# Kernel optimization log

Hardware: AMD Instinct MI355X
Metric: run time of the kernel (lower is better)

The kernel has to match this reference:

```python
import jax, jax.numpy as jnp
import numpy as np

THRESHOLD = 0.3
STRENGTH = 0.1
MIN_S = 0.0
MAX_S = 0.5
EPS_COS = 1e-8
EPS_LN = 1e-5

B, T, D = 1024, 64, 256
P = 2048
H = 512


def _layernorm(x, g, b):
    mu = x.mean(-1, keepdims=True)
    var = ((x - mu) ** 2).mean(-1, keepdims=True)
    return (x - mu) * jax.lax.rsqrt(var + EPS_LN) * g + b


def setup_inputs() -> dict:
    key = jax.random.key(0)
    ks = jax.random.split(key, 10)
    s = lambda fan_in: 1.0 / np.sqrt(fan_in)
    return {
        "current_feat": jax.random.normal(ks[0], (B, T, D), jnp.float32),
        "prototype": jax.random.normal(ks[1], (P, T, D), jnp.float32),
        "dd_w1": jax.random.normal(ks[2], (2 * D, H), jnp.float32) * s(2 * D),
        "dd_b1": jnp.zeros((H,), jnp.float32),
        "dd_g1": jnp.ones((H,), jnp.float32),
        "dd_be1": jnp.zeros((H,), jnp.float32),
        "dd_w2": jax.random.normal(ks[3], (H, H // 2), jnp.float32) * s(H),
        "dd_b2": jnp.zeros((H // 2,), jnp.float32),
        "dd_w3": jax.random.normal(ks[4], (H // 2, 1), jnp.float32) * s(H // 2),
        "dd_b3": jnp.zeros((1,), jnp.float32),
        "cal_w1": jax.random.normal(ks[5], (D, H), jnp.float32) * s(D),
        "cal_b1": jnp.zeros((H,), jnp.float32),
        "cal_g1": jnp.ones((H,), jnp.float32),
        "cal_be1": jnp.zeros((H,), jnp.float32),
        "cal_w2": jax.random.normal(ks[6], (H, H), jnp.float32) * s(H),
        "cal_b2": jnp.zeros((H,), jnp.float32),
        "cal_w3": jax.random.normal(ks[7], (H, D), jnp.float32) * s(H),
        "cal_b3": jnp.zeros((D,), jnp.float32),
    }


def reference(current_feat, prototype,
              dd_w1, dd_b1, dd_g1, dd_be1, dd_w2, dd_b2, dd_w3, dd_b3,
              cal_w1, cal_b1, cal_g1, cal_be1, cal_w2, cal_b2, cal_w3, cal_b3):
    # --- drift detection ---
    feat_flat = current_feat.mean(axis=1)          # [B, D]
    proto_centers = prototype.mean(axis=1)         # [P, D]
    fn = jnp.maximum(jnp.linalg.norm(feat_flat, axis=-1), EPS_COS)   # [B]
    pn = jnp.maximum(jnp.linalg.norm(proto_centers, axis=-1), EPS_COS)  # [P]
    sim = jnp.einsum('bd,pd->bp', feat_flat, proto_centers) / (fn[:, None] * pn[None, :])
    drift_score = 1.0 - sim                        # [B, P]
    is_drifted = drift_score.mean(axis=0) > THRESHOLD  # [P] bool

    # --- calibration (batched over all P, then masked scatter) ---
    global_mean = feat_flat.mean(axis=0)           # [D]
    concat = jnp.concatenate(
        [proto_centers, jnp.broadcast_to(global_mean, (proto_centers.shape[0], global_mean.shape[0]))], axis=-1)  # [P, 2D]
    h = jax.nn.relu(_layernorm(concat @ dd_w1 + dd_b1, dd_g1, dd_be1))
    h = jax.nn.relu(h @ dd_w2 + dd_b2)
    drift_conf = jax.nn.sigmoid(h @ dd_w3 + dd_b3)[:, 0]  # [P]

    c = jax.nn.relu(_layernorm(proto_centers @ cal_w1 + cal_b1, cal_g1, cal_be1))
    c = jax.nn.relu(c @ cal_w2 + cal_b2)
    delta = c @ cal_w3 + cal_b3                    # [P, D]

    strength = jnp.clip(STRENGTH * drift_conf, MIN_S, MAX_S)  # [P]
    new_center = proto_centers + strength[:, None] * delta    # [P, D]

    calibrated = jnp.where(is_drifted[:, None, None], new_center[:, None, :], prototype)  # [P, T, D]
    return calibrated, drift_score, is_drifted
```

## Files before the change

kernel.cpp:

```cpp
#include <hip/hip_runtime.h>
#include <hip/hip_bf16.h>
#include <math.h>

#define BB 1024
#define TT 64
#define DD 256
#define PP 2048
#define HH 512

typedef __attribute__((ext_vector_type(8))) short short8;
typedef __attribute__((ext_vector_type(4))) float f32x4;

__device__ __forceinline__ float blk_reduce(float v, float* sm) {
    int tid = threadIdx.x;
    #pragma unroll
    for (int o = 32; o > 0; o >>= 1) v += __shfl_down(v, o, 64);
    if ((tid & 63) == 0) sm[tid >> 6] = v;
    __syncthreads();
    float r = sm[0] + sm[1] + sm[2] + sm[3];
    __syncthreads();
    return r;
}

__device__ __forceinline__ float row_mean_vec(const float* __restrict__ base,
                                              float* __restrict__ smr) {
    int tid = threadIdx.x;
    int c4 = tid & 63;
    int t0 = tid >> 6;
    float4 s = make_float4(0.f, 0.f, 0.f, 0.f);
    #pragma unroll
    for (int t = t0; t < TT; t += 4) {
        float4 v = *(const float4*)(base + t * DD + (c4 << 2));
        s.x += v.x; s.y += v.y; s.z += v.z; s.w += v.w;
    }
    *(float4*)&smr[t0 * 256 + (c4 << 2)] = s;
    __syncthreads();
    float m = (smr[tid] + smr[256 + tid] + smr[512 + tid] + smr[768 + tid]) * (1.f / TT);
    __syncthreads();
    return m;
}

__global__ void prep_k(const float* __restrict__ cf, const float* __restrict__ proto,
                       const float* __restrict__ dd_w1, const float* __restrict__ dd_w2,
                       const float* __restrict__ cal_w1, const float* __restrict__ cal_w2,
                       const float* __restrict__ cal_w3,
                       float* __restrict__ gmean8, float* __restrict__ fn,
                       float* __restrict__ pn, float* __restrict__ pc,
                       __hip_bfloat16* __restrict__ ffb, __hip_bfloat16* __restrict__ pcb,
                       __hip_bfloat16* __restrict__ w1cat, __hip_bfloat16* __restrict__ w2dd,
                       __hip_bfloat16* __restrict__ w2cal, __hip_bfloat16* __restrict__ w3cal) {
    __shared__ float smr[1024];
    __shared__ float sm[4];
    int b = blockIdx.x, tid = threadIdx.x;
    if (b < 1024) {
        float m = row_mean_vec(cf + (size_t)b * TT * DD, smr);
        ffb[(size_t)b * DD + tid] = __float2bfloat16(m);
        atomicAdd(&gmean8[(b & 7) * 256 + tid], m * (1.f / BB));
        float tot = blk_reduce(m * m, sm);
        if (tid == 0) fn[b] = fmaxf(sqrtf(tot), 1e-8f);
    } else if (b < 3072) {
        int r = b - 1024;
        float m = row_mean_vec(proto + (size_t)r * TT * DD, smr);
        pc[(size_t)r * DD + tid] = m;
        pcb[(size_t)r * DD + tid] = __float2bfloat16(m);
        float tot = blk_reduce(m * m, sm);
        if (tid == 0) pn[r] = fmaxf(sqrtf(tot), 1e-8f);
    } else {
        int idx = (b - 3072) * 256 + tid;
        if (idx < 262144) {
            int half = idx >> 17;
            int i = idx & 131071;
            int n = i & 511, k = i >> 9;
            const float* src = half ? cal_w1 : dd_w1;
            w1cat[(size_t)(half * 512 + n) * 256 + k] = __float2bfloat16(src[(size_t)k * 512 + n]);
        } else if (idx < 393216) {
            int i = idx - 262144;
            int n = i & 255, k = i >> 8;
            w2dd[(size_t)n * 512 + k] = __float2bfloat16(dd_w2[(size_t)k * 256 + n]);
        } else if (idx < 655360) {
            int i = idx - 393216;
            int n = i & 511, k = i >> 9;
            w2cal[(size_t)n * 512 + k] = __float2bfloat16(cal_w2[(size_t)k * 512 + n]);
        } else {
            int i = idx - 655360;
            int n = i & 255, k = i >> 8;
            w3cal[(size_t)n * 512 + k] = __float2bfloat16(cal_w3[(size_t)k * 256 + n]);
        }
    }
}

__global__ void sim_addvec_k(const __hip_bfloat16* __restrict__ A,
                             const __hip_bfloat16* __restrict__ Bt,
                             const float* __restrict__ fn, const float* __restrict__ pn,
                             const float* __restrict__ gmean8,
                             const float* __restrict__ dd_w1, const float* __restrict__ dd_b1,
                             float* __restrict__ drift, float* __restrict__ colsum,
                             float* __restrict__ addvec) {
    if (blockIdx.x >= 512) {
        __shared__ float gmk[256];
        int tid = threadIdx.x;
        float g = 0.f;
        #pragma unroll
        for (int s = 0; s < 8; ++s) g += gmean8[s * 256 + tid];
        gmk[tid] = g;
        __syncthreads();
        int j = (blockIdx.x - 512) * 256 + tid;
        float s = dd_b1[j];
        #pragma unroll 8
        for (int k = 0; k < 256; ++k) s = fmaf(gmk[k], dd_w1[(size_t)(256 + k) * 512 + j], s);
        addvec[j] = s;
        return;
    }
    int wid = (blockIdx.x << 2) + (threadIdx.x >> 6);
    int lane = threadIdx.x & 63;
    int mw = wid >> 6, nw = wid & 63;
    int m0 = mw << 5, n0 = nw << 5;
    int lr = lane & 15, quad = lane >> 4;
    const __hip_bfloat16* pa0 = A + (size_t)(m0 + lr) * DD + quad * 8;
    const __hip_bfloat16* pa1 = pa0 + 16 * DD;
    const __hip_bfloat16* pb0 = Bt + (size_t)(n0 + lr) * DD + quad * 8;
    const __hip_bfloat16* pb1 = pb0 + 16 * DD;
    f32x4 acc00 = {0,0,0,0}, acc01 = {0,0,0,0}, acc10 = {0,0,0,0}, acc11 = {0,0,0,0};
    #pragma unroll
    for (int k = 0; k < DD; k += 32) {
        short8 a0 = *(const short8*)(pa0 + k);
        short8 a1 = *(const short8*)(pa1 + k);
        short8 b0 = *(const short8*)(pb0 + k);
        short8 b1 = *(const short8*)(pb1 + k);
        acc00 = __builtin_amdgcn_mfma_f32_16x16x32_bf16(a0, b0, acc00, 0, 0, 0);
        acc01 = __builtin_amdgcn_mfma_f32_16x16x32_bf16(a0, b1, acc01, 0, 0, 0);
        acc10 = __builtin_amdgcn_mfma_f32_16x16x32_bf16(a1, b0, acc10, 0, 0, 0);
        acc11 = __builtin_amdgcn_mfma_f32_16x16x32_bf16(a1, b1, acc11, 0, 0, 0);
    }
    int col0 = n0 + lr, col1 = col0 + 16;
    float ip0 = 1.f / pn[col0], ip1 = 1.f / pn[col1];
    float cs0 = 0.f, cs1 = 0.f;
    #pragma unroll
    for (int r = 0; r < 4; ++r) {
        int row0 = m0 + quad * 4 + r;
        int row1 = row0 + 16;
        float if0 = 1.f / fn[row0];
        float if1 = 1.f / fn[row1];
        float d00 = 1.f - acc00[r] * if0 * ip0;
        float d01 = 1.f - acc01[r] * if0 * ip1;
        float d10 = 1.f - acc10[r] * if1 * ip0;
        float d11 = 1.f - acc11[r] * if1 * ip1;
        drift[(size_t)row0 * PP + col0] = d00;
        drift[(size_t)row0 * PP + col1] = d01;
        drift[(size_t)row1 * PP + col0] = d10;
        drift[(size_t)row1 * PP + col1] = d11;
        cs0 += d00 + d10;
        cs1 += d01 + d11;
    }
    cs0 += __shfl_xor(cs0, 16, 64); cs0 += __shfl_xor(cs0, 32, 64);
    cs1 += __shfl_xor(cs1, 16, 64); cs1 += __shfl_xor(cs1, 32, 64);
    if (quad == 0) {
        atomicAdd(&colsum[col0], cs0);
        atomicAdd(&colsum[col1], cs1);
    }
}

template <int K, int OUT_BF16, int RELU>
__device__ __forceinline__ void gemm_tile(const __hip_bfloat16* __restrict__ A,
                                          const __hip_bfloat16* __restrict__ Bt,
                                          const float* __restrict__ bias0,
                                          const float* __restrict__ bias1, int split,
                                          void* __restrict__ Cout, int N, int lognt,
                                          int wid, int lane) {
    int mw = wid >> lognt, nw = wid & ((1 << lognt) - 1);
    int m0 = mw << 5, n0 = nw << 5;
    int lr = lane & 15, quad = lane >> 4;
    const __hip_bfloat16* pa0 = A + (size_t)(m0 + lr) * K + quad * 8;
    const __hip_bfloat16* pa1 = pa0 + 16 * K;
    const __hip_bfloat16* pb0 = Bt + (size_t)(n0 + lr) * K + quad * 8;
    const __hip_bfloat16* pb1 = pb0 + 16 * K;
    f32x4 acc00 = {0,0,0,0}, acc01 = {0,0,0,0}, acc10 = {0,0,0,0}, acc11 = {0,0,0,0};
    #pragma unroll
    for (int k = 0; k < K; k += 32) {
        short8 a0 = *(const short8*)(pa0 + k);
        short8 a1 = *(const short8*)(pa1 + k);
        short8 b0 = *(const short8*)(pb0 + k);
        short8 b1 = *(const short8*)(pb1 + k);
        acc00 = __builtin_amdgcn_mfma_f32_16x16x32_bf16(a0, b0, acc00, 0, 0, 0);
        acc01 = __builtin_amdgcn_mfma_f32_16x16x32_bf16(a0, b1, acc01, 0, 0, 0);
        acc10 = __builtin_amdgcn_mfma_f32_16x16x32_bf16(a1, b0, acc10, 0, 0, 0);
        acc11 = __builtin_amdgcn_mfma_f32_16x16x32_bf16(a1, b1, acc11, 0, 0, 0);
    }
    int col0 = n0 + lr, col1 = col0 + 16;
    float bi0 = (col0 < split) ? bias0[col0] : bias1[col0 - split];
    float bi1 = (col1 < split) ? bias0[col1] : bias1[col1 - split];
    #pragma unroll
    for (int r = 0; r < 4; ++r) {
        int row0 = m0 + quad * 4 + r;
        int row1 = row0 + 16;
        float v00 = acc00[r] + bi0, v01 = acc01[r] + bi1;
        float v10 = acc10[r] + bi0, v11 = acc11[r] + bi1;
        if (RELU) {
            v00 = fmaxf(v00, 0.f); v01 = fmaxf(v01, 0.f);
            v10 = fmaxf(v10, 0.f); v11 = fmaxf(v11, 0.f);
        }
        if (OUT_BF16) {
            __hip_bfloat16* C = (__hip_bfloat16*)Cout;
            C[(size_t)row0 * N + col0] = __float2bfloat16(v00);
            C[(size_t)row0 * N + col1] = __float2bfloat16(v01);
            C[(size_t)row1 * N + col0] = __float2bfloat16(v10);
            C[(size_t)row1 * N + col1] = __float2bfloat16(v11);
        } else {
            float* C = (float*)Cout;
            C[(size_t)row0 * N + col0] = v00;
            C[(size_t)row0 * N + col1] = v01;
            C[(size_t)row1 * N + col0] = v10;
            C[(size_t)row1 * N + col1] = v11;
        }
    }
}

__global__ void gemm1_k(const __hip_bfloat16* __restrict__ pcb,
                        const __hip_bfloat16* __restrict__ w1cat,
                        const float* __restrict__ addvec, const float* __restrict__ cal_b1,
                        float* __restrict__ buf1) {
    int wid = (blockIdx.x << 2) + (threadIdx.x >> 6);
    gemm_tile<256, 0, 0>(pcb, w1cat, addvec, cal_b1, 512, buf1, 1024, 5,
                         wid, threadIdx.x & 63);
}

__global__ void ln2_k(const float* __restrict__ X,
                      __hip_bfloat16* __restrict__ Ydd, __hip_bfloat16* __restrict__ Ycal,
                      const float* __restrict__ gdd, const float* __restrict__ bedd,
                      const float* __restrict__ gcal, const float* __restrict__ becal) {
    __shared__ float sm[4];
    int r = blockIdx.x, tid = threadIdx.x;
    const float* row = X + (size_t)r * 1024;
    {
        float x0 = row[tid], x1 = row[tid + 256];
        float mu = blk_reduce(x0 + x1, sm) * (1.f / HH);
        float d0 = x0 - mu, d1 = x1 - mu;
        float var = blk_reduce(d0 * d0 + d1 * d1, sm) * (1.f / HH);
        float rs = rsqrtf(var + 1e-5f);
        __hip_bfloat16* y = Ydd + (size_t)r * HH;
        y[tid]       = __float2bfloat16(fmaxf(d0 * rs * gdd[tid] + bedd[tid], 0.f));
        y[tid + 256] = __float2bfloat16(fmaxf(d1 * rs * gdd[tid + 256] + bedd[tid + 256], 0.f));
    }
    {
        float x0 = row[512 + tid], x1 = row[768 + tid];
        float mu = blk_reduce(x0 + x1, sm) * (1.f / HH);
        float d0 = x0 - mu, d1 = x1 - mu;
        float var = blk_reduce(d0 * d0 + d1 * d1, sm) * (1.f / HH);
        float rs = rsqrtf(var + 1e-5f);
        __hip_bfloat16* y = Ycal + (size_t)r * HH;
        y[tid]       = __float2bfloat16(fmaxf(d0 * rs * gcal[tid] + becal[tid], 0.f));
        y[tid + 256] = __float2bfloat16(fmaxf(d1 * rs * gcal[tid + 256] + becal[tid + 256], 0.f));
    }
}

__global__ void gemm2_k(const __hip_bfloat16* __restrict__ act_dd,
                        const __hip_bfloat16* __restrict__ act_cal,
                        const __hip_bfloat16* __restrict__ w2dd,
                        const __hip_bfloat16* __restrict__ w2cal,
                        const float* __restrict__ dd_b2, const float* __restrict__ cal_b2,
                        __hip_bfloat16* __restrict__ act2b, __hip_bfloat16* __restrict__ act3b) {
    int lane = threadIdx.x & 63;
    if (blockIdx.x < 128) {
        int wid = (blockIdx.x << 2) + (threadIdx.x >> 6);
        gemm_tile<512, 1, 1>(act_dd, w2dd, dd_b2, dd_b2, 1 << 30, act2b, 256, 3, wid, lane);
    } else {
        int wid = ((blockIdx.x - 128) << 2) + (threadIdx.x >> 6);
        gemm_tile<512, 1, 1>(act_cal, w2cal, cal_b2, cal_b2, 1 << 30, act3b, 512, 4, wid, lane);
    }
}

__global__ void gemm3_conf_k(const __hip_bfloat16* __restrict__ act3b,
                             const __hip_bfloat16* __restrict__ w3cal,
                             const float* __restrict__ cal_b3,
                             const __hip_bfloat16* __restrict__ act2b,
                             const float* __restrict__ dd_w3, const float* __restrict__ dd_b3,
                             const float* __restrict__ colsum,
                             float* __restrict__ delta, float* __restrict__ strength,
                             float* __restrict__ out_is) {
    if (blockIdx.x < 128) {
        int wid = (blockIdx.x << 2) + (threadIdx.x >> 6);
        gemm_tile<512, 0, 0>(act3b, w3cal, cal_b3, cal_b3, 1 << 30, delta, 256, 3,
                             wid, threadIdx.x & 63);
        return;
    }
    int p = ((blockIdx.x - 128) << 2) + (threadIdx.x >> 6);
    int lane = threadIdx.x & 63;
    const __hip_bfloat16* row = act2b + (size_t)p * 256 + lane * 4;
    float s = 0.f;
    #pragma unroll
    for (int j = 0; j < 4; ++j)
        s += __bfloat162float(row[j]) * dd_w3[lane * 4 + j];
    #pragma unroll
    for (int o = 32; o > 0; o >>= 1) s += __shfl_down(s, o, 64);
    if (lane == 0) {
        float conf = 1.f / (1.f + expf(-(s + dd_b3[0])));
        strength[p] = fminf(fmaxf(0.1f * conf, 0.f), 0.5f);
        out_is[p] = (colsum[p] * (1.f / BB) > 0.3f) ? 1.f : 0.f;
    }
}

__global__ void finalize_k(const float* __restrict__ pc, const float* __restrict__ delta,
                           const float* __restrict__ strength, const float* __restrict__ colsum,
                           const float* __restrict__ proto, float* __restrict__ out) {
    int p = blockIdx.x;
    int d4 = (threadIdx.x & 63) << 2;
    int t0 = threadIdx.x >> 6;
    bool dr = colsum[p] * (1.f / BB) > 0.3f;
    float* o = out + (size_t)p * TT * DD;
    if (dr) {
        float s = strength[p];
        float4 pcv = *(const float4*)(pc + (size_t)p * DD + d4);
        float4 dv  = *(const float4*)(delta + (size_t)p * DD + d4);
        float4 nc = make_float4(fmaf(s, dv.x, pcv.x), fmaf(s, dv.y, pcv.y),
                                fmaf(s, dv.z, pcv.z), fmaf(s, dv.w, pcv.w));
        #pragma unroll
        for (int t = t0; t < TT; t += 4)
            *(float4*)(o + t * DD + d4) = nc;
    } else {
        const float* pr = proto + (size_t)p * TT * DD;
        #pragma unroll
        for (int t = t0; t < TT; t += 4)
            *(float4*)(o + t * DD + d4) = *(const float4*)(pr + t * DD + d4);
    }
}

extern "C" void kernel_launch(void* const* d_in, const int* in_sizes, int n_in,
                              void* d_out, int out_size, void* d_ws, size_t ws_size,
                              hipStream_t stream) {
    const float* cf     = (const float*)d_in[0];
    const float* proto  = (const float*)d_in[1];
    const float* dd_w1  = (const float*)d_in[2];
    const float* dd_b1  = (const float*)d_in[3];
    const float* dd_g1  = (const float*)d_in[4];
    const float* dd_be1 = (const float*)d_in[5];
    const float* dd_w2  = (const float*)d_in[6];
    const float* dd_b2  = (const float*)d_in[7];
    const float* dd_w3  = (const float*)d_in[8];
    const float* dd_b3  = (const float*)d_in[9];
    const float* cal_w1 = (const float*)d_in[10];
    const float* cal_b1 = (const float*)d_in[11];
    const float* cal_g1 = (const float*)d_in[12];
    const float* cal_be1= (const float*)d_in[13];
    const float* cal_w2 = (const float*)d_in[14];
    const float* cal_b2 = (const float*)d_in[15];
    const float* cal_w3 = (const float*)d_in[16];
    const float* cal_b3 = (const float*)d_in[17];

    float* out_cal   = (float*)d_out;
    float* out_drift = out_cal + (size_t)PP * TT * DD;
    float* out_is    = out_drift + (size_t)BB * PP;

    float* w = (float*)d_ws;
    float* gmean8   = w;
    float* colsum   = w + 2048;
    float* addvec   = w + 4096;
    float* fn       = w + 4608;
    float* pn       = w + 5632;
    float* strength = w + 7680;
    float* pc       = w + 9728;
    float* buf1     = w + 534016;
    float* delta    = w + 2631168;
    __hip_bfloat16* bb = (__hip_bfloat16*)(w + 3155456);
    __hip_bfloat16* ffb     = bb;
    __hip_bfloat16* pcb     = bb + 262144;
    __hip_bfloat16* w1cat   = bb + 786432;
    __hip_bfloat16* w2dd    = bb + 1048576;
    __hip_bfloat16* w2cal   = bb + 1179648;
    __hip_bfloat16* w3cal   = bb + 1441792;
    __hip_bfloat16* act_dd  = bb + 1572864;
    __hip_bfloat16* act_cal = bb + 2621440;
    __hip_bfloat16* act2b   = bb + 3670016;
    __hip_bfloat16* act3b   = bb + 4194304;

    hipMemsetAsync(d_ws, 0, 4096 * sizeof(float), stream);

    prep_k<<<6144, 256, 0, stream>>>(cf, proto, dd_w1, dd_w2, cal_w1, cal_w2, cal_w3,
                                     gmean8, fn, pn, pc, ffb, pcb,
                                     w1cat, w2dd, w2cal, w3cal);
    sim_addvec_k<<<514, 256, 0, stream>>>(ffb, pcb, fn, pn, gmean8, dd_w1, dd_b1,
                                          out_drift, colsum, addvec);
    gemm1_k<<<512, 256, 0, stream>>>(pcb, w1cat, addvec, cal_b1, buf1);
    ln2_k<<<PP, 256, 0, stream>>>(buf1, act_dd, act_cal, dd_g1, dd_be1, cal_g1, cal_be1);
    gemm2_k<<<384, 256, 0, stream>>>(act_dd, act_cal, w2dd, w2cal, dd_b2, cal_b2,
                                     act2b, act3b);
    gemm3_conf_k<<<640, 256, 0, stream>>>(act3b, w3cal, cal_b3, act2b, dd_w3, dd_b3,
                                          colsum, delta, strength, out_is);
    finalize_k<<<PP, 256, 0, stream>>>(pc, delta, strength, colsum, proto, out_cal);
}
```

Measured before the change: 415.7 us.

## Batch row-mean loads, drop gmean atomics, use nontemporal stores, single-pass LayerNorm

Row-mean loads are issued all at once (16 float4 per thread) to raise memory-level parallelism. The global-mean atomics are replaced by storing per-row means and having the addvec blocks reduce them directly. Drift and calibrated-output writes become nontemporal stores to avoid polluting cache. LayerNorm now computes mean and variance in one fused reduction (E[x^2]-mu^2), which is slightly less numerically stable. Together these cut atomic traffic, sync points and cache pressure in a bandwidth-bound pipeline.

Measured after the change: 410.2 us. No clear change (-1.3%).

```diff
diff --git a/kernel.cpp b/kernel.cpp
--- a/kernel.cpp
+++ b/kernel.cpp
@@ -10,6 +10,19 @@
 
 typedef __attribute__((ext_vector_type(8))) short short8;
 typedef __attribute__((ext_vector_type(4))) float f32x4;
+
+__device__ __forceinline__ float4 f4add(float4 a, float4 b) {
+    return make_float4(a.x + b.x, a.y + b.y, a.z + b.z, a.w + b.w);
+}
+
+__device__ __forceinline__ void nt_store4(float* p, float4 v) {
+    f32x4 t = {v.x, v.y, v.z, v.w};
+    __builtin_nontemporal_store(t, (f32x4*)p);
+}
+
+__device__ __forceinline__ void nt_store1(float* p, float v) {
+    __builtin_nontemporal_store(v, p);
+}
 
 __device__ __forceinline__ float blk_reduce(float v, float* sm) {
     int tid = threadIdx.x;
@@ -22,29 +35,46 @@
     return r;
 }
 
-__device__ __forceinline__ float row_mean_vec(const float* __restrict__ base,
-                                              float* __restrict__ smr) {
+__device__ __forceinline__ float2 blk_reduce2(float a, float b, float* sm) {
+    int tid = threadIdx.x;
+    #pragma unroll
+    for (int o = 32; o > 0; o >>= 1) {
+        a += __shfl_down(a, o, 64);
+        b += __shfl_down(b, o, 64);
+    }
+    if ((tid & 63) == 0) { sm[(tid >> 6) * 2] = a; sm[(tid >> 6) * 2 + 1] = b; }
+    __syncthreads();
+    float ra = sm[0] + sm[2] + sm[4] + sm[6];
+    float rb = sm[1] + sm[3] + sm[5] + sm[7];
+    __syncthreads();
+    return make_float2(ra, rb);
+}
+
+__device__ __forceinline__ float row_mean_batch(const float* __restrict__ base,
+                                                float* __restrict__ smr) {
     int tid = threadIdx.x;
     int c4 = tid & 63;
     int t0 = tid >> 6;
-    float4 s = make_float4(0.f, 0.f, 0.f, 0.f);
-    #pragma unroll
-    for (int t = t0; t < TT; t += 4) {
-        float4 v = *(const float4*)(base + t * DD + (c4 << 2));
-        s.x += v.x; s.y += v.y; s.z += v.z; s.w += v.w;
-    }
+    const float* p = base + t0 * DD + (c4 << 2);
+    float4 v[16];
+    #pragma unroll
+    for (int i = 0; i < 16; ++i)
+        v[i] = *(const float4*)(p + (i << 2) * DD);
+    #pragma unroll
+    for (int i = 0; i < 8; ++i) v[i] = f4add(v[i], v[i + 8]);
+    #pragma unroll
+    for (int i = 0; i < 4; ++i) v[i] = f4add(v[i], v[i + 4]);
+    float4 s = f4add(f4add(v[0], v[1]), f4add(v[2], v[3]));
     *(float4*)&smr[t0 * 256 + (c4 << 2)] = s;
     __syncthreads();
-    float m = (smr[tid] + smr[256 + tid] + smr[512 + tid] + smr[768 + tid]) * (1.f / TT);
-    __syncthreads();
-    return m;
+    return (smr[tid] + smr[256 + tid] + smr[512 + tid] + smr[768 + tid]) * (1.f / TT);
 }
 
 __global__ void prep_k(const float* __restrict__ cf, const float* __restrict__ proto,
                        const float* __restrict__ dd_w1, const float* __restrict__ dd_w2,
                        const float* __restrict__ cal_w1, const float* __restrict__ cal_w2,
                        const float* __restrict__ cal_w3,
-                       float* __restrict__ gmean8, float* __restrict__ fn,
+                       float* __restrict__ ffm, float* __restrict__ fn,
                        float* __restrict__ pn, float* __restrict__ pc,
                        __hip_bfloat16* __restrict__ ffb, __hip_bfloat16* __restrict__ pcb,
                        __hip_bfloat16* __restrict__ w1cat, __hip_bfloat16* __restrict__ w2dd,
@@ -53,18 +83,26 @@
     __shared__ float sm[4];
     int b = blockIdx.x, tid = threadIdx.x;
     if (b < 1024) {
-        float m = row_mean_vec(cf + (size_t)b * TT * DD, smr);
+        float m = row_mean_batch(cf + (size_t)b * TT * DD, smr);
+        ffm[(size_t)b * DD + tid] = m;
         ffb[(size_t)b * DD + tid] = __float2bfloat16(m);
-        atomicAdd(&gmean8[(b & 7) * 256 + tid], m * (1.f / BB));
-        float tot = blk_reduce(m * m, sm);
-        if (tid == 0) fn[b] = fmaxf(sqrtf(tot), 1e-8f);
+        float q = m * m;
+        #pragma unroll
+        for (int o = 32; o > 0; o >>= 1) q += __shfl_down(q, o, 64);
+        if ((tid & 63) == 0) sm[tid >> 6] = q;
+        __syncthreads();
+        if (tid == 0) fn[b] = fmaxf(sqrtf(sm[0] + sm[1] + sm[2] + sm[3]), 1e-8f);
     } else if (b < 3072) {
         int r = b - 1024;
-        float m = row_mean_vec(proto + (size_t)r * TT * DD, smr);
+        float m = row_mean_batch(proto + (size_t)r * TT * DD, smr);
         pc[(size_t)r * DD + tid] = m;
         pcb[(size_t)r * DD + tid] = __float2bfloat16(m);
-        float tot = blk_reduce(m * m, sm);
-        if (tid == 0) pn[r] = fmaxf(sqrtf(tot), 1e-8f);
+        float q = m * m;
+        #pragma unroll
+        for (int o = 32; o > 0; o >>= 1) q += __shfl_down(q, o, 64);
+        if ((tid & 63) == 0) sm[tid >> 6] = q;
+        __syncthreads();
+        if (tid == 0) pn[r] = fmaxf(sqrtf(sm[0] + sm[1] + sm[2] + sm[3]), 1e-8f);
     } else {
         int idx = (b - 3072) * 256 + tid;
         if (idx < 262144) {
@@ -92,17 +130,23 @@
 __global__ void sim_addvec_k(const __hip_bfloat16* __restrict__ A,
                              const __hip_bfloat16* __restrict__ Bt,
                              const float* __restrict__ fn, const float* __restrict__ pn,
-                             const float* __restrict__ gmean8,
+                             const float* __restrict__ ffm,
                              const float* __restrict__ dd_w1, const float* __restrict__ dd_b1,
                              float* __restrict__ drift, float* __restrict__ colsum,
                              float* __restrict__ addvec) {
     if (blockIdx.x >= 512) {
         __shared__ float gmk[256];
         int tid = threadIdx.x;
-        float g = 0.f;
-        #pragma unroll
-        for (int s = 0; s < 8; ++s) g += gmean8[s * 256 + tid];
-        gmk[tid] = g;
+        const float* f = ffm + tid;
+        float a0 = 0.f, a1 = 0.f, a2 = 0.f, a3 = 0.f, a4 = 0.f, a5 = 0.f, a6 = 0.f, a7 = 0.f;
+        #pragma unroll 4
+        for (int b = 0; b < 1024; b += 8) {
+            a0 += f[(b + 0) << 8]; a1 += f[(b + 1) << 8];
+            a2 += f[(b + 2) << 8]; a3 += f[(b + 3) << 8];
+            a4 += f[(b + 4) << 8]; a5 += f[(b + 5) << 8];
+            a6 += f[(b + 6) << 8]; a7 += f[(b + 7) << 8];
+        }
+        gmk[tid] = (((a0 + a1) + (a2 + a3)) + ((a4 + a5) + (a6 + a7))) * (1.f / BB);
         __syncthreads();
         int j = (blockIdx.x - 512) * 256 + tid;
         float s = dd_b1[j];
@@ -145,10 +189,10 @@
         float d01 = 1.f - acc01[r] * if0 * ip1;
         float d10 = 1.f - acc10[r] * if1 * ip0;
         float d11 = 1.f - acc11[r] * if1 * ip1;
-        drift[(size_t)row0 * PP + col0] = d00;
-        drift[(size_t)row0 * PP + col1] = d01;
-        drift[(size_t)row1 * PP + col0] = d10;
-        drift[(size_t)row1 * PP + col1] = d11;
+        nt_store1(&drift[(size_t)row0 * PP + col0], d00);
+        nt_store1(&drift[(size_t)row0 * PP + col1], d01);
+        nt_store1(&drift[(size_t)row1 * PP + col0], d10);
+        nt_store1(&drift[(size_t)row1 * PP + col1], d11);
         cs0 += d00 + d10;
         cs1 += d01 + d11;
     }
@@ -228,25 +272,27 @@
                       __hip_bfloat16* __restrict__ Ydd, __hip_bfloat16* __restrict__ Ycal,
                       const float* __restrict__ gdd, const float* __restrict__ bedd,
                       const float* __restrict__ gcal, const float* __restrict__ becal) {
-    __shared__ float sm[4];
+    __shared__ float sm[8];
     int r = blockIdx.x, tid = threadIdx.x;
     const float* row = X + (size_t)r * 1024;
     {
         float x0 = row[tid], x1 = row[tid + 256];
-        float mu = blk_reduce(x0 + x1, sm) * (1.f / HH);
+        float2 t = blk_reduce2(x0 + x1, x0 * x0 + x1 * x1, sm);
+        float mu = t.x * (1.f / HH);
+        float var = fmaxf(t.y * (1.f / HH) - mu * mu, 0.f);
+        float rs = rsqrtf(var + 1e-5f);
         float d0 = x0 - mu, d1 = x1 - mu;
-        float var = blk_reduce(d0 * d0 + d1 * d1, sm) * (1.f / HH);
-        float rs = rsqrtf(var + 1e-5f);
         __hip_bfloat16* y = Ydd + (size_t)r * HH;
         y[tid]       = __float2bfloat16(fmaxf(d0 * rs * gdd[tid] + bedd[tid], 0.f));
         y[tid + 256] = __float2bfloat16(fmaxf(d1 * rs * gdd[tid + 256] + bedd[tid + 256], 0.f));
     }
     {
         float x0 = row[512 + tid], x1 = row[768 + tid];
-        float mu = blk_reduce(x0 + x1, sm) * (1.f / HH);
+        float2 t = blk_reduce2(x0 + x1, x0 * x0 + x1 * x1, sm);
+        float mu = t.x * (1.f / HH);
+        float var = fmaxf(t.y * (1.f / HH) - mu * mu, 0.f);
+        float rs = rsqrtf(var + 1e-5f);
         float d0 = x0 - mu, d1 = x1 - mu;
-        float var = blk_reduce(d0 * d0 + d1 * d1, sm) * (1.f / HH);
-        float rs = rsqrtf(var + 1e-5f);
         __hip_bfloat16* y = Ycal + (size_t)r * HH;
         y[tid]       = __float2bfloat16(fmaxf(d0 * rs * gcal[tid] + becal[tid], 0.f));
         y[tid + 256] = __float2bfloat16(fmaxf(d1 * rs * gcal[tid + 256] + becal[tid + 256], 0.f));
@@ -315,12 +361,12 @@
                                 fmaf(s, dv.z, pcv.z), fmaf(s, dv.w, pcv.w));
         #pragma unroll
         for (int t = t0; t < TT; t += 4)
-            *(float4*)(o + t * DD + d4) = nc;
+            nt_store4(o + t * DD + d4, nc);
     } else {
         const float* pr = proto + (size_t)p * TT * DD;
         #pragma unroll
         for (int t = t0; t < TT; t += 4)
-            *(float4*)(o + t * DD + d4) = *(const float4*)(pr + t * DD + d4);
+            nt_store4(o + t * DD + d4, *(const float4*)(pr + t * DD + d4));
     }
 }
 
@@ -351,14 +397,14 @@
     float* out_is    = out_drift + (size_t)BB * PP;
 
     float* w = (float*)d_ws;
-    float* gmean8   = w;
-    float* colsum   = w + 2048;
+    float* colsum   = w;
     float* addvec   = w + 4096;
     float* fn       = w + 4608;
     float* pn       = w + 5632;
     float* strength = w + 7680;
     float* pc       = w + 9728;
     float* buf1     = w + 534016;
+    float* ffm      = buf1;
     float* delta    = w + 2631168;
     __hip_bfloat16* bb = (__hip_bfloat16*)(w + 3155456);
     __hip_bfloat16* ffb     = bb;
@@ -372,12 +418,12 @@
     __hip_bfloat16* act2b   = bb + 3670016;
     __hip_bfloat16* act3b   = bb + 4194304;
 
-    hipMemsetAsync(d_ws, 0, 4096 * sizeof(float), stream);
+    hipMemsetAsync(colsum, 0, 2048 * sizeof(float), stream);
 
     prep_k<<<6144, 256, 0, stream>>>(cf, proto, dd_w1, dd_w2, cal_w1, cal_w2, cal_w3,
-                                     gmean8, fn, pn, pc, ffb, pcb,
+                                     ffm, fn, pn, pc, ffb, pcb,
                                      w1cat, w2dd, w2cal, w3cal);
-    sim_addvec_k<<<514, 256, 0, stream>>>(ffb, pcb, fn, pn, gmean8, dd_w1, dd_b1,
+    sim_addvec_k<<<514, 256, 0, stream>>>(ffb, pcb, fn, pn, ffm, dd_w1, dd_b1,
                                           out_drift, colsum, addvec);
     gemm1_k<<<512, 256, 0, stream>>>(pcb, w1cat, addvec, cal_b1, buf1);
     ln2_k<<<PP, 256, 0, stream>>>(buf1, act_dd, act_cal, dd_g1, dd_be1, cal_g1, cal_be1);
```
